# Kernel optimization log

Measured on AMD Instinct MI355X. Metric: run time of the kernel, lower is better.

## Reference

```python
import jax, jax.numpy as jnp
import numpy as np

B, IN, H, T = 512, 256, 128, 100

def _build_norm_adj():
    # Hardcoded topology from GraphConvLSTM.build_graph (22 nodes, cliques per sublist)
    adj_list = [[0, 2, 5, 8, 11], [0, 1, 4, 7, 10], [0, 3, 6, 9, 12, 15],
                [9, 14, 17, 19, 21], [9, 13, 16, 18, 20]]
    n = max(max(s) for s in adj_list) + 1  # 22
    A = np.zeros((n, n), dtype=np.float32)
    for s in adj_list:
        for i in range(len(s)):
            for j in range(i + 1, len(s)):
                A[s[i], s[j]] = 1.0
                A[s[j], s[i]] = 1.0
    # DGL GraphConv norm='both': D^{-1/2} A D^{-1/2} (degrees clamped to >=1)
    deg = np.clip(A.sum(axis=1), 1.0, None)
    dinv = 1.0 / np.sqrt(deg)
    return jnp.asarray(dinv[:, None] * A * dinv[None, :])  # (N, N)

A_NORM = _build_norm_adj()
N = A_NORM.shape[0]  # 22

def setup_inputs() -> dict:
    key = jax.random.key(0)
    ks = jax.random.split(key, 11)
    s_in = 1.0 / np.sqrt(IN)
    s_h = 1.0 / np.sqrt(H)
    return {
        "x":     jax.random.normal(ks[0], (B, IN), jnp.float32),
        "wi_w":  jax.random.normal(ks[1], (H, IN), jnp.float32) * s_in,
        "wi_b":  jax.random.normal(ks[2], (H,), jnp.float32) * s_in,
        "wf_w":  jax.random.normal(ks[3], (H, IN), jnp.float32) * s_in,
        "wf_b":  jax.random.normal(ks[4], (H,), jnp.float32) * s_in,
        "wo_w":  jax.random.normal(ks[5], (H, IN), jnp.float32) * s_in,
        "wo_b":  jax.random.normal(ks[6], (H,), jnp.float32) * s_in,
        "wc_w":  jax.random.normal(ks[7], (H, IN), jnp.float32) * s_in,
        "wc_b":  jax.random.normal(ks[8], (H,), jnp.float32) * s_in,
        "gcn_w": jax.random.normal(ks[9], (H, H), jnp.float32) * s_h,
        "gcn_b": jax.random.normal(ks[10], (H,), jnp.float32) * s_h,
    }

def reference(x, wi_w, wi_b, wf_w, wf_b, wo_w, wo_b, wc_w, wc_b, gcn_w, gcn_b):
    # x is fixed across timesteps in the original forward -> project gates once.
    xi = (x @ wi_w.T + wi_b)[:, None, :]  # (B,1,H) broadcast over nodes
    xf = (x @ wf_w.T + wf_b)[:, None, :]
    xo = (x @ wo_w.T + wo_b)[:, None, :]
    xc = (x @ wc_w.T + wc_b)[:, None, :]

    def step(carry, _):
        h, c = carry
        # All four gates share the identical gcn_h(g, h_prev) result.
        msg = jnp.einsum('mn,bnh->bmh', A_NORM, h)  # (B,N,H)
        g = msg @ gcn_w + gcn_b
        i_t = jax.nn.sigmoid(xi + g)
        f_t = jax.nn.sigmoid(xf + g)
        o_t = jax.nn.sigmoid(xo + g)
        c_til = jnp.tanh(xc + g)
        c_t = f_t * c + i_t * c_til
        h_t = o_t * jnp.tanh(c_t)
        return (h_t, c_t), h_t

    h0 = jnp.zeros((B, N, H), x.dtype)
    c0 = jnp.zeros((B, N, H), x.dtype)
    _, hs = jax.lax.scan(step, (h0, c0), None, length=T)  # (T,B,N,H)
    out = jnp.transpose(hs, (1, 0, 2, 3)).reshape(B, -1)  # (B, T*N*H)
    return out
```

## Files before the change

### kernel.cpp

```cpp
#include <hip/hip_runtime.h>
#include <hip/hip_bf16.h>
#include <math.h>


#define B_   512
#define IN_  256
#define H_   128
#define T_   100
#define N_   22
#define NH   (N_ * H_)
#define TNH  (T_ * NH)
#define HP   136
#define THREADS 512

typedef __attribute__((ext_vector_type(8))) _Float16 half8_t;
typedef __attribute__((ext_vector_type(4))) float f32x4;

__device__ __forceinline__ float sigm(float x) {
    float e = __builtin_exp2f(x * -1.442695041f);
    return __builtin_amdgcn_rcpf(1.0f + e);
}
__device__ __forceinline__ float tanh_f(float x) {
    float a = fabsf(x);
    float e = __builtin_exp2f(a * -2.885390082f);
    float r = (1.0f - e) * __builtin_amdgcn_rcpf(1.0f + e);
    return copysignf(r, x);
}

__global__ void __launch_bounds__(THREADS, 4)
gclstm_kernel(const float* __restrict__ x,
              const float* __restrict__ wi_w, const float* __restrict__ wi_b,
              const float* __restrict__ wf_w, const float* __restrict__ wf_b,
              const float* __restrict__ wo_w, const float* __restrict__ wo_b,
              const float* __restrict__ wc_w, const float* __restrict__ wc_b,
              const float* __restrict__ gcn_w, const float* __restrict__ gcn_b,
              float* __restrict__ out)
{
    __shared__ __align__(16) _Float16 h_hi[32][HP];
    __shared__ __align__(16) _Float16 h_lo[32][HP];
    __shared__ __align__(16) float hw_lds[N_][H_ + 1];
    __shared__ float xp_lds[4][H_];
    __shared__ __align__(16) float xrow[IN_];

    const int t    = threadIdx.x;
    const int b    = blockIdx.x;
    const int ho   = t & (H_ - 1);
    const int mg   = t >> 7;
    const int wid  = t >> 6;
    const int lane = t & 63;
    const int lrow = lane & 15;
    const int lkg  = lane >> 4;

    if (t < IN_ / 4) {
        reinterpret_cast<float4*>(xrow)[t] =
            reinterpret_cast<const float4*>(x + (size_t)b * IN_)[t];
    }
    for (int e = t; e < 32 * HP / 2; e += THREADS) ((int*)h_hi)[e] = 0;
    for (int e = t; e < 32 * HP / 2; e += THREADS) ((int*)h_lo)[e] = 0;
    __syncthreads();

    {
        const float* wg = (mg == 0) ? wi_w : (mg == 1) ? wf_w : (mg == 2) ? wo_w : wc_w;
        const float* bg = (mg == 0) ? wi_b : (mg == 1) ? wf_b : (mg == 2) ? wo_b : wc_b;
        const float* rg = wg + (size_t)ho * IN_;
        float acc = bg[ho];
        #pragma unroll
        for (int k4 = 0; k4 < IN_ / 4; ++k4) {
            float4 xv = reinterpret_cast<const float4*>(xrow)[k4];
            float4 wv = reinterpret_cast<const float4*>(rg)[k4];
            acc += wv.x * xv.x + wv.y * xv.y + wv.z * xv.z + wv.w * xv.w;
        }
        xp_lds[mg][ho] = acc;
    }

    half8_t Wf[4];
    #pragma unroll
    for (int ks = 0; ks < 4; ++ks) {
        #pragma unroll
        for (int i = 0; i < 8; ++i) {
            const int k   = 32 * ks + 8 * lkg + i;
            const int col = 16 * wid + lrow;
            Wf[ks][i] = (_Float16)gcn_w[k * H_ + col];
        }
    }
    __syncthreads();

    const float gb   = gcn_b[ho];
    const float xi_r = xp_lds[0][ho] + gb;
    const float xf_r = xp_lds[1][ho] + gb;
    const float xo_r = xp_lds[2][ho] + gb;
    const float xc_r = xp_lds[3][ho] + gb;

    float c_reg[6];
    #pragma unroll
    for (int i = 0; i < 6; ++i) c_reg[i] = 0.0f;

    float* outb = out + (size_t)b * TNH + ho;

    #define D13 0.2773500981126146f
    #define D5  0.4472135954999579f
    #define D4  0.5f
    const float DINV[22] = {D13, D4, D4, D5, D4, D4, D5, D4, D4, D13, D4,
                            D4,  D5, D4, D4, D5, D4, D4, D4, D4, D4,  D4};

    for (int step = 0; step < T_; ++step) {
        f32x4 acc0 = (f32x4)(0.0f);
        f32x4 acc1 = (f32x4)(0.0f);

        #pragma unroll
        for (int ks = 0; ks < 4; ++ks) {
            const int ko = 32 * ks + 8 * lkg;
            const half8_t Ah0 = *reinterpret_cast<const half8_t*>(&h_hi[lrow][ko]);
            const half8_t Ah1 = *reinterpret_cast<const half8_t*>(&h_hi[16 + lrow][ko]);
            const half8_t Al0 = *reinterpret_cast<const half8_t*>(&h_lo[lrow][ko]);
            const half8_t Al1 = *reinterpret_cast<const half8_t*>(&h_lo[16 + lrow][ko]);
            acc0 = __builtin_amdgcn_mfma_f32_16x16x32_f16(Ah0, Wf[ks], acc0, 0, 0, 0);
            acc0 = __builtin_amdgcn_mfma_f32_16x16x32_f16(Al0, Wf[ks], acc0, 0, 0, 0);
            acc1 = __builtin_amdgcn_mfma_f32_16x16x32_f16(Ah1, Wf[ks], acc1, 0, 0, 0);
            acc1 = __builtin_amdgcn_mfma_f32_16x16x32_f16(Al1, Wf[ks], acc1, 0, 0, 0);
        }
        #pragma unroll
        for (int i = 0; i < 4; ++i) {
            const int row = 4 * lkg + i;
            hw_lds[row][16 * wid + lrow] = acc0[i];
            const int row2 = 16 + row;
            if (row2 < N_) hw_lds[row2][16 * wid + lrow] = acc1[i];
        }
        __syncthreads();

        float tt[22];
        #pragma unroll
        for (int m = 0; m < 22; ++m) tt[m] = DINV[m] * hw_lds[m][ho];

        const float S0 = tt[0] + tt[2] + tt[5] + tt[8] + tt[11];
        const float S1 = tt[0] + tt[1] + tt[4] + tt[7] + tt[10];
        const float S2 = tt[0] + tt[3] + tt[6] + tt[9] + tt[12] + tt[15];
        const float S3 = tt[9] + tt[14] + tt[17] + tt[19] + tt[21];
        const float S4 = tt[9] + tt[13] + tt[16] + tt[18] + tt[20];

        float* outs = outb + (size_t)step * NH;

        #define UPD(n, nn, SSexpr, KK) {                                        \
            const float g  = DINV[n] * ((SSexpr) - (KK) * tt[n]);               \
            const float it = sigm(xi_r + g);                                    \
            const float ft = sigm(xf_r + g);                                    \
            const float ot = sigm(xo_r + g);                                    \
            const float ct = tanh_f(xc_r + g);                                  \
            const float cn = ft * c_reg[nn] + it * ct;                          \
            c_reg[nn] = cn;                                                     \
            const float hn = ot * tanh_f(cn);                                   \
            outs[(n) * H_] = hn;                                                \
            const _Float16 hh = (_Float16)hn;                                   \
            h_hi[n][ho] = hh;                                                   \
            h_lo[n][ho] = (_Float16)(hn - (float)hh);                           \
        }

        if (mg == 0) {
            UPD(0, 0, S0 + S1 + S2, 3.0f)
            UPD(1, 1, S1, 1.0f)
            UPD(2, 2, S0, 1.0f)
            UPD(3, 3, S2, 1.0f)
            UPD(4, 4, S1, 1.0f)
            UPD(5, 5, S0, 1.0f)
        } else if (mg == 1) {
            UPD(6, 0, S2, 1.0f)
            UPD(7, 1, S1, 1.0f)
            UPD(8, 2, S0, 1.0f)
            UPD(9, 3, S2 + S3 + S4, 3.0f)
            UPD(10, 4, S1, 1.0f)
        } else if (mg == 2) {
            UPD(11, 0, S0, 1.0f)
            UPD(12, 1, S2, 1.0f)
            UPD(13, 2, S4, 1.0f)
            UPD(14, 3, S3, 1.0f)
            UPD(15, 4, S2, 1.0f)
            UPD(16, 5, S4, 1.0f)
        } else {
            UPD(17, 0, S3, 1.0f)
            UPD(18, 1, S4, 1.0f)
            UPD(19, 2, S3, 1.0f)
            UPD(20, 3, S4, 1.0f)
            UPD(21, 4, S3, 1.0f)
        }
        #undef UPD
        __syncthreads();
    }
}

extern "C" void kernel_launch(void* const* d_in, const int* in_sizes, int n_in,
                              void* d_out, int out_size, void* d_ws, size_t ws_size,
                              hipStream_t stream) {
    const float* x     = (const float*)d_in[0];
    const float* wi_w  = (const float*)d_in[1];
    const float* wi_b  = (const float*)d_in[2];
    const float* wf_w  = (const float*)d_in[3];
    const float* wf_b  = (const float*)d_in[4];
    const float* wo_w  = (const float*)d_in[5];
    const float* wo_b  = (const float*)d_in[6];
    const float* wc_w  = (const float*)d_in[7];
    const float* wc_b  = (const float*)d_in[8];
    const float* gcn_w = (const float*)d_in[9];
    const float* gcn_b = (const float*)d_in[10];
    float* out = (float*)d_out;

    gclstm_kernel<<<dim3(B_), dim3(THREADS), 0, stream>>>(
        x, wi_w, wi_b, wf_w, wf_b, wo_w, wo_b, wc_w, wc_b, gcn_w, gcn_b, out);
}
```

Before: 902.1 us.

## Use 32x32 MFMA, transposed swizzled LDS staging, and shared-exp gate activations

New measurement: 794.5 us. 1.14x faster.

```diff
diff --git a/kernel.cpp b/kernel.cpp
--- a/kernel.cpp
+++ b/kernel.cpp
@@ -12,20 +12,10 @@
 #define TNH  (T_ * NH)
 #define HP   136
 #define THREADS 512
-
-typedef __attribute__((ext_vector_type(8))) _Float16 half8_t;
-typedef __attribute__((ext_vector_type(4))) float f32x4;
-
-__device__ __forceinline__ float sigm(float x) {
-    float e = __builtin_exp2f(x * -1.442695041f);
-    return __builtin_amdgcn_rcpf(1.0f + e);
-}
-__device__ __forceinline__ float tanh_f(float x) {
-    float a = fabsf(x);
-    float e = __builtin_exp2f(a * -2.885390082f);
-    float r = (1.0f - e) * __builtin_amdgcn_rcpf(1.0f + e);
-    return copysignf(r, x);
-}
+#define LOG2E 1.442695041f
+
+typedef __attribute__((ext_vector_type(8)))  _Float16 half8_t;
+typedef __attribute__((ext_vector_type(16))) float    f32x16;
 
 __global__ void __launch_bounds__(THREADS, 4)
 gclstm_kernel(const float* __restrict__ x,
@@ -38,18 +28,18 @@
 {
     __shared__ __align__(16) _Float16 h_hi[32][HP];
     __shared__ __align__(16) _Float16 h_lo[32][HP];
-    __shared__ __align__(16) float hw_lds[N_][H_ + 1];
+    __shared__ __align__(16) float    hw_T[H_ * 32];
     __shared__ float xp_lds[4][H_];
     __shared__ __align__(16) float xrow[IN_];
 
-    const int t    = threadIdx.x;
-    const int b    = blockIdx.x;
-    const int ho   = t & (H_ - 1);
-    const int mg   = t >> 7;
-    const int wid  = t >> 6;
-    const int lane = t & 63;
-    const int lrow = lane & 15;
-    const int lkg  = lane >> 4;
+    const int t     = threadIdx.x;
+    const int b     = blockIdx.x;
+    const int ho    = t & (H_ - 1);
+    const int mg    = t >> 7;
+    const int wid   = t >> 6;
+    const int lane  = t & 63;
+    const int l31   = lane & 31;
+    const int khalf = lane >> 5;
 
     if (t < IN_ / 4) {
         reinterpret_cast<float4*>(xrow)[t] =
@@ -73,14 +63,15 @@
         xp_lds[mg][ho] = acc;
     }
 
-    half8_t Wf[4];
-    #pragma unroll
-    for (int ks = 0; ks < 4; ++ks) {
-        #pragma unroll
-        for (int i = 0; i < 8; ++i) {
-            const int k   = 32 * ks + 8 * lkg + i;
-            const int col = 16 * wid + lrow;
-            Wf[ks][i] = (_Float16)gcn_w[k * H_ + col];
+    half8_t Bf[8];
+    if (wid < 4) {
+        const int col = 32 * wid + l31;
+        #pragma unroll
+        for (int kk = 0; kk < 8; ++kk) {
+            #pragma unroll
+            for (int i = 0; i < 8; ++i) {
+                Bf[kk][i] = (_Float16)gcn_w[(16 * kk + 8 * khalf + i) * H_ + col];
+            }
         }
     }
     __syncthreads();
@@ -90,6 +81,10 @@
     const float xf_r = xp_lds[1][ho] + gb;
     const float xo_r = xp_lds[2][ho] + gb;
     const float xc_r = xp_lds[3][ho] + gb;
+    const float Ei   = __builtin_exp2f(-LOG2E * xi_r);
+    const float Ef   = __builtin_exp2f(-LOG2E * xf_r);
+    const float Eo   = __builtin_exp2f(-LOG2E * xo_r);
+    const float E2c  = __builtin_exp2f(-2.0f * LOG2E * xc_r);
 
     float c_reg[6];
     #pragma unroll
@@ -104,33 +99,37 @@
                             D4,  D5, D4, D4, D5, D4, D4, D4, D4, D4,  D4};
 
     for (int step = 0; step < T_; ++step) {
-        f32x4 acc0 = (f32x4)(0.0f);
-        f32x4 acc1 = (f32x4)(0.0f);
-
-        #pragma unroll
-        for (int ks = 0; ks < 4; ++ks) {
-            const int ko = 32 * ks + 8 * lkg;
-            const half8_t Ah0 = *reinterpret_cast<const half8_t*>(&h_hi[lrow][ko]);
-            const half8_t Ah1 = *reinterpret_cast<const half8_t*>(&h_hi[16 + lrow][ko]);
-            const half8_t Al0 = *reinterpret_cast<const half8_t*>(&h_lo[lrow][ko]);
-            const half8_t Al1 = *reinterpret_cast<const half8_t*>(&h_lo[16 + lrow][ko]);
-            acc0 = __builtin_amdgcn_mfma_f32_16x16x32_f16(Ah0, Wf[ks], acc0, 0, 0, 0);
-            acc0 = __builtin_amdgcn_mfma_f32_16x16x32_f16(Al0, Wf[ks], acc0, 0, 0, 0);
-            acc1 = __builtin_amdgcn_mfma_f32_16x16x32_f16(Ah1, Wf[ks], acc1, 0, 0, 0);
-            acc1 = __builtin_amdgcn_mfma_f32_16x16x32_f16(Al1, Wf[ks], acc1, 0, 0, 0);
-        }
-        #pragma unroll
-        for (int i = 0; i < 4; ++i) {
-            const int row = 4 * lkg + i;
-            hw_lds[row][16 * wid + lrow] = acc0[i];
-            const int row2 = 16 + row;
-            if (row2 < N_) hw_lds[row2][16 * wid + lrow] = acc1[i];
+        if (wid < 4) {
+            f32x16 acc = (f32x16)(0.0f);
+            #pragma unroll
+            for (int kk = 0; kk < 8; ++kk) {
+                const int ko = 16 * kk + 8 * khalf;
+                const half8_t Ah = *reinterpret_cast<const half8_t*>(&h_hi[l31][ko]);
+                const half8_t Al = *reinterpret_cast<const half8_t*>(&h_lo[l31][ko]);
+                acc = __builtin_amdgcn_mfma_f32_32x32x16_f16(Ah, Bf[kk], acc, 0, 0, 0);
+                acc = __builtin_amdgcn_mfma_f32_32x32x16_f16(Al, Bf[kk], acc, 0, 0, 0);
+            }
+            const int col = 32 * wid + l31;
+            #pragma unroll
+            for (int q = 0; q < 4; ++q) {
+                float4 v = make_float4(acc[4 * q], acc[4 * q + 1],
+                                       acc[4 * q + 2], acc[4 * q + 3]);
+                const int unit = (2 * q + khalf) ^ (col & 7);
+                *reinterpret_cast<float4*>(&hw_T[col * 32 + unit * 4]) = v;
+            }
         }
         __syncthreads();
 
-        float tt[22];
-        #pragma unroll
-        for (int m = 0; m < 22; ++m) tt[m] = DINV[m] * hw_lds[m][ho];
+        float tt[24];
+        #pragma unroll
+        for (int u = 0; u < 6; ++u) {
+            const int unit = u ^ (ho & 7);
+            float4 v = *reinterpret_cast<const float4*>(&hw_T[ho * 32 + unit * 4]);
+            tt[4 * u + 0] = v.x; tt[4 * u + 1] = v.y;
+            tt[4 * u + 2] = v.z; tt[4 * u + 3] = v.w;
+        }
+        #pragma unroll
+        for (int m = 0; m < 22; ++m) tt[m] *= DINV[m];
 
         const float S0 = tt[0] + tt[2] + tt[5] + tt[8] + tt[11];
         const float S1 = tt[0] + tt[1] + tt[4] + tt[7] + tt[10];
@@ -141,14 +140,18 @@
         float* outs = outb + (size_t)step * NH;
 
         #define UPD(n, nn, SSexpr, KK) {                                        \
-            const float g  = DINV[n] * ((SSexpr) - (KK) * tt[n]);               \
-            const float it = sigm(xi_r + g);                                    \
-            const float ft = sigm(xf_r + g);                                    \
-            const float ot = sigm(xo_r + g);                                    \
-            const float ct = tanh_f(xc_r + g);                                  \
-            const float cn = ft * c_reg[nn] + it * ct;                          \
+            const float g   = DINV[n] * ((SSexpr) - (KK) * tt[n]);              \
+            const float E   = __builtin_exp2f(-LOG2E * g);                      \
+            const float it  = __builtin_amdgcn_rcpf(1.0f + E * Ei);             \
+            const float ft  = __builtin_amdgcn_rcpf(1.0f + E * Ef);             \
+            const float ot  = __builtin_amdgcn_rcpf(1.0f + E * Eo);             \
+            const float e2  = fminf(E * E * E2c, 1e30f);                        \
+            const float ct  = (1.0f - e2) * __builtin_amdgcn_rcpf(1.0f + e2);   \
+            const float cn  = ft * c_reg[nn] + it * ct;                         \
             c_reg[nn] = cn;                                                     \
-            const float hn = ot * tanh_f(cn);                                   \
+            const float e2n = fminf(__builtin_exp2f(-2.0f * LOG2E * cn), 1e30f);\
+            const float th  = (1.0f - e2n) * __builtin_amdgcn_rcpf(1.0f + e2n); \
+            const float hn  = ot * th;                                          \
             outs[(n) * H_] = hn;                                                \
             const _Float16 hh = (_Float16)hn;                                   \
             h_hi[n][ho] = hh;                                                   \
```
